# Kernel optimization log

Hardware: AMD Instinct MI355X
Metric: run time of the kernel (lower is better)

## Reference

```python
import jax, jax.numpy as jnp
import numpy as np

B, N, F, D, TOPK, EXTRA = 32, 128, 10, 64, 20, 25
BN = B * N
EPS = 1e-5
SLOPE = 0.2  # GDN GraphLayer leaky_relu negative slope


def _cosine(a, b):
    na = jnp.maximum(jnp.linalg.norm(a, axis=-1), 1e-12)
    nb = jnp.maximum(jnp.linalg.norm(b, axis=-1), 1e-12)
    return (a @ b.T) / (na[:, None] * nb[None, :])


def _segment_softmax(logits, seg, num):
    m = jax.ops.segment_max(logits, seg, num_segments=num)
    m = jnp.where(jnp.isfinite(m), m, 0.0)  # empty segments
    e = jnp.exp(logits - m[seg])
    s = jax.ops.segment_sum(e, seg, num_segments=num)
    return e / jnp.maximum(s[seg], 1e-12)


def setup_inputs() -> dict:
    key = jax.random.key(0)
    ks = jax.random.split(key, 12)
    r = lambda i, shape, s=1.0: jax.random.normal(ks[i], shape, dtype=jnp.float32) * s
    return dict(
        data=r(0, (B, N, F)),
        emb=r(1, (N, D)) * 0.3,                       # nn.Embedding(node_num, dim)
        W1=r(2, (F, D)) * (1.0 / np.sqrt(F)),         # GraphLayer lin
        att_i1=r(3, (2 * D,)) * 0.1,                  # att on concat(h, emb)
        att_j1=r(4, (2 * D,)) * 0.1,
        bias1=jnp.zeros((D,), jnp.float32),
        bn1_g=jnp.ones((D,), jnp.float32),
        bn1_b=jnp.zeros((D,), jnp.float32),
        P=r(5, (BN, BN)) * (1.0 / np.sqrt(BN)),       # extra_pram
        W2=r(6, (D, D)) * (1.0 / np.sqrt(D)),         # GraphLayer1 lin
        att_i2=r(7, (D,)) * 0.1,
        att_j2=r(8, (D,)) * 0.1,
        bias2=jnp.zeros((D,), jnp.float32),
        bnO_g=jnp.ones((D,), jnp.float32),
        bnO_b=jnp.zeros((D,), jnp.float32),
        W_out=r(9, (D, 1)) * (1.0 / np.sqrt(D)),      # OutLayer Linear(dim,1)
        b_out=jnp.zeros((1,), jnp.float32),
        org_edge_index=jnp.zeros((2, 2), jnp.int32),  # dead arg in original forward
    )


def _forward(data, emb, W1, att_i1, att_j1, bias1, bn1_g, bn1_b, P, W2,
             att_i2, att_j2, bias2, bnO_g, bnO_b, W_out, b_out):
    x = data.reshape(BN, F)

    # ---- learned top-k graph from detached embedding cosine similarity ----
    w = jax.lax.stop_gradient(emb)              # weights_arr = detach()
    cos = _cosine(w, w)                         # [N, N]
    topv, topi = jax.lax.top_k(cos, TOPK)       # [N, TOPK]
    cos_w = jnp.tile(topv.reshape(-1), B)       # [B*N*TOPK]
    src0 = topi.reshape(-1)                     # gated_j (source)
    dst0 = jnp.repeat(jnp.arange(N), TOPK)      # gated_i (target)
    offs = jnp.repeat(jnp.arange(B) * N, N * TOPK)
    src = jnp.tile(src0, B) + offs
    dst = jnp.tile(dst0, B) + offs

    # ---- GraphLayer (GAT-style with embedding keys, edge weight = cos) ----
    all_emb = jnp.tile(emb, (B, 1))             # [BN, D]
    h = x @ W1                                  # [BN, D]
    kf = jnp.concatenate([h, all_emb], axis=-1) # [BN, 2D]
    si, sj = kf @ att_i1, kf @ att_j1           # [BN]
    score = jax.nn.leaky_relu(si[dst] + sj[src], SLOPE) * cos_w
    alpha = _segment_softmax(score, dst, BN)
    agg = jax.ops.segment_sum(h[src] * alpha[:, None], dst, num_segments=BN) + bias1
    mu, var = agg.mean(0), agg.var(0)           # BatchNorm1d (batch stats)
    gcn = jax.nn.relu(bn1_g * (agg - mu) / jnp.sqrt(var + EPS) + bn1_b)

    # ---- extra-feature branch (always taken: P is [BN, BN]) ----
    ef = P.T @ gcn                              # (gcn_out.T @ P).T
    g = jnp.concatenate([gcn, ef], axis=0)      # [2BN, D]
    cos2 = _cosine(g, g)                        # [2BN, 2BN]
    topv2, topi2 = jax.lax.top_k(cos2, EXTRA)
    corrs = topv2[:BN].reshape(-1)              # [BN*EXTRA]
    src2 = jnp.repeat(jnp.arange(BN), EXTRA)    # extra_i = edge_index[0] (source)
    dst2 = topi2[:BN].reshape(-1)               # extra_j = edge_index[1] (target)

    # ---- GraphLayer1 (no embedding keys, no BN in GNNLayer1.forward) ----
    h2 = g @ W2                                 # [2BN, D]
    s2 = jax.nn.leaky_relu((h2 @ att_i2)[dst2] + (h2 @ att_j2)[src2], SLOPE) * corrs
    alpha2 = _segment_softmax(s2, dst2, 2 * BN)
    agg2 = jax.ops.segment_sum(h2[src2] * alpha2[:, None], dst2, num_segments=2 * BN) + bias2
    gcn2 = jax.nn.relu(agg2)[:BN]

    # ---- output head: mul by embedding, BN over channels, Linear(D,1) ----
    x3 = gcn2.reshape(B, N, D) * emb[None]      # [B, N, D]
    mu2, var2 = x3.mean((0, 1)), x3.var((0, 1)) # BatchNorm1d over channel D
    x4 = jax.nn.relu(bnO_g * (x3 - mu2) / jnp.sqrt(var2 + EPS) + bnO_b)
    out = x4 @ W_out + b_out                    # [B, N, 1]; dropout = identity (eval)
    return out.reshape(-1, N)                   # [B, N]


def reference(data, emb, W1, att_i1, att_j1, bias1, bn1_g, bn1_b, P, W2,
              att_i2, att_j2, bias2, bnO_g, bnO_b, W_out, b_out, org_edge_index):
    # org_edge_index is dead in the original forward (only cached, never consumed)
    return _forward(data, emb, W1, att_i1, att_j1, bias1, bn1_g, bn1_b, P, W2,
                    att_i2, att_j2, bias2, bnO_g, bnO_b, W_out, b_out)
```

## Files before the change

kernel.cpp:

```cpp
#include <hip/hip_runtime.h>
#include <hip/hip_bf16.h>
#include <math.h>

#define DEV __device__ __forceinline__

constexpr int Bb   = 32;
constexpr int Nn   = 128;
constexpr int Ff   = 10;
constexpr int Dd   = 64;
constexpr int TOPK = 20;
constexpr int EXTRA= 25;
constexpr int BN   = 4096;
constexpr int TBN  = 8192;
constexpr int RC   = 16;
constexpr int CAND_CAP = 1024;
constexpr float EPS   = 1e-5f;
constexpr float SLOPE = 0.2f;

DEV unsigned int fenc(float f){
  unsigned int b = __float_as_uint(f);
  return (b & 0x80000000u) ? ~b : (b | 0x80000000u);
}
DEV float fdec(unsigned int u){
  unsigned int b = (u & 0x80000000u) ? (u & 0x7FFFFFFFu) : ~u;
  return __uint_as_float(b);
}

__global__ void k_zero(float* __restrict__ p, int n){
  int i = blockIdx.x*256 + threadIdx.x;
  if(i < n) p[i] = 0.f;
}

__global__ void k_emb_norm(const float* __restrict__ emb, float* __restrict__ norms){
  int i = blockIdx.x, d = threadIdx.x;
  float v = emb[i*Dd + d];
  float s = v*v;
  for(int o=32;o>0;o>>=1) s += __shfl_down(s, o, 64);
  if(d==0) norms[i] = fmaxf(sqrtf(s), 1e-12f);
}

__global__ void k_emb_topk(const float* __restrict__ emb, const float* __restrict__ norms,
                           float* __restrict__ topv, int* __restrict__ topi){
  __shared__ float se[Dd];
  __shared__ float sc[Nn];
  __shared__ float rv[Nn];
  __shared__ int   ri[Nn];
  int i = blockIdx.x, t = threadIdx.x;
  if(t < Dd) se[t] = emb[i*Dd + t];
  __syncthreads();
  float dot = 0.f;
  for(int d=0; d<Dd; d++) dot += se[d]*emb[t*Dd + d];
  sc[t] = dot/(norms[i]*norms[t]);
  __syncthreads();
  for(int k=0; k<TOPK; k++){
    rv[t] = sc[t]; ri[t] = t; __syncthreads();
    for(int o=Nn/2; o>0; o>>=1){
      if(t < o){
        float v2 = rv[t+o]; int i2 = ri[t+o];
        if(v2 > rv[t] || (v2 == rv[t] && i2 < ri[t])){ rv[t]=v2; ri[t]=i2; }
      }
      __syncthreads();
    }
    if(t==0){
      topv[i*TOPK + k] = rv[0];
      topi[i*TOPK + k] = ri[0];
      sc[ri[0]] = -INFINITY;
    }
    __syncthreads();
  }
}

__global__ void k_h1(const float* __restrict__ data, const float* __restrict__ emb,
                     const float* __restrict__ W1, const float* __restrict__ ai1,
                     const float* __restrict__ aj1,
                     float* __restrict__ h, float* __restrict__ si, float* __restrict__ sj){
  int r = blockIdx.x, d = threadIdx.x;
  int node = r & (Nn-1);
  __shared__ float xr[Ff];
  if(d < Ff) xr[d] = data[r*Ff + d];
  __syncthreads();
  float hv = 0.f;
  #pragma unroll
  for(int f=0; f<Ff; f++) hv += xr[f]*W1[f*Dd + d];
  h[r*Dd + d] = hv;
  float e = emb[node*Dd + d];
  float a = hv*ai1[d] + e*ai1[Dd + d];
  float b = hv*aj1[d] + e*aj1[Dd + d];
  for(int o=32;o>0;o>>=1){ a += __shfl_down(a,o,64); b += __shfl_down(b,o,64); }
  if(d==0){ si[r] = a; sj[r] = b; }
}

__global__ void k_agg1(const float* __restrict__ h, const float* __restrict__ si,
                       const float* __restrict__ sj, const float* __restrict__ topv,
                       const int* __restrict__ topi, const float* __restrict__ bias1,
                       float* __restrict__ agg){
  int r = blockIdx.x, d = threadIdx.x;
  int b = r >> 7, node = r & (Nn-1);
  __shared__ float sal[TOPK];
  __shared__ int   ssrc[TOPK];
  if(d < TOPK){
    int s = b*Nn + topi[node*TOPK + d];
    float sc = si[r] + sj[s];
    sc = sc >= 0.f ? sc : SLOPE*sc;
    sal[d] = sc * topv[node*TOPK + d];
    ssrc[d] = s;
  }
  __syncthreads();
  float m = -INFINITY;
  #pragma unroll
  for(int k=0;k<TOPK;k++) m = fmaxf(m, sal[k]);
  float al[TOPK]; float ssum = 0.f;
  #pragma unroll
  for(int k=0;k<TOPK;k++){ al[k] = expf(sal[k]-m); ssum += al[k]; }
  float inv = 1.0f/fmaxf(ssum, 1e-12f);
  float acc = 0.f;
  #pragma unroll
  for(int k=0;k<TOPK;k++) acc += al[k]*inv*h[ssrc[k]*Dd + d];
  agg[r*Dd + d] = acc + bias1[d];
}

__global__ void k_colstats(const float* __restrict__ x, float* __restrict__ mu, float* __restrict__ var){
  int c = blockIdx.x, t = threadIdx.x;
  float s = 0.f, s2 = 0.f;
  for(int r=t; r<BN; r+=256){ float v = x[r*Dd + c]; s += v; s2 += v*v; }
  __shared__ float ls[256], ls2[256];
  ls[t]=s; ls2[t]=s2; __syncthreads();
  for(int o=128;o>0;o>>=1){
    if(t<o){ ls[t]+=ls[t+o]; ls2[t]+=ls2[t+o]; }
    __syncthreads();
  }
  if(t==0){ float m = ls[0]/BN; mu[c]=m; var[c]=ls2[0]/BN - m*m; }
}

__global__ void k_bnrelu1(const float* __restrict__ agg, const float* __restrict__ mu,
                          const float* __restrict__ var, const float* __restrict__ gamma,
                          const float* __restrict__ beta, float* __restrict__ g){
  int idx = blockIdx.x*256 + threadIdx.x;
  int c = idx & (Dd-1);
  float v = agg[idx];
  float y = gamma[c]*(v - mu[c])/sqrtf(var[c]+EPS) + beta[c];
  g[idx] = fmaxf(y, 0.f);
}

__global__ __launch_bounds__(256) void k_ef1(const float* __restrict__ P, const float* __restrict__ gcn,
                                             float* __restrict__ part){
  __shared__ float Pt[16*64];
  __shared__ float Gt[16*64];
  int t = threadIdx.x;
  int jbase = blockIdx.x*64;
  int r0 = blockIdx.y*256;
  int row = t >> 4, col4 = (t & 15)*4;
  int tr = t >> 4, tc = t & 15;
  float acc[4][4] = {};
  for(int step=0; step<16; step++){
    int r = r0 + step*16;
    float4 pv = *(const float4*)&P[(size_t)(r+row)*BN + jbase + col4];
    float4 gv = *(const float4*)&gcn[(r+row)*Dd + col4];
    __syncthreads();
    *(float4*)&Pt[row*64 + col4] = pv;
    *(float4*)&Gt[row*64 + col4] = gv;
    __syncthreads();
    #pragma unroll
    for(int rr=0; rr<16; rr++){
      float4 pa = *(float4*)&Pt[rr*64 + tr*4];
      float4 gb = *(float4*)&Gt[rr*64 + tc*4];
      float pav[4] = {pa.x, pa.y, pa.z, pa.w};
      float gbv[4] = {gb.x, gb.y, gb.z, gb.w};
      #pragma unroll
      for(int a=0;a<4;a++)
        #pragma unroll
        for(int b=0;b<4;b++) acc[a][b] += pav[a]*gbv[b];
    }
  }
  float* dst = part + ((size_t)blockIdx.y*BN + jbase)*Dd;
  #pragma unroll
  for(int a=0;a<4;a++){
    float4 v = make_float4(acc[a][0],acc[a][1],acc[a][2],acc[a][3]);
    *(float4*)&dst[(tr*4+a)*Dd + tc*4] = v;
  }
}

__global__ void k_ef2(const float* __restrict__ part, float* __restrict__ ef){
  int i = blockIdx.x*256 + threadIdx.x;
  float4 s = make_float4(0.f,0.f,0.f,0.f);
  #pragma unroll
  for(int c=0;c<RC;c++){
    float4 v = *(const float4*)&part[(size_t)c*BN*Dd + (size_t)i*4];
    s.x += v.x; s.y += v.y; s.z += v.z; s.w += v.w;
  }
  *(float4*)&ef[(size_t)i*4] = s;
}

__global__ void k_rownorm(const float* __restrict__ x, float* __restrict__ nrm){
  int r = blockIdx.x, d = threadIdx.x;
  float v = x[(size_t)r*Dd + d];
  float s = v*v;
  for(int o=32;o>0;o>>=1) s += __shfl_down(s, o, 64);
  if(d==0) nrm[r] = fmaxf(sqrtf(s), 1e-12f);
}

__global__ __launch_bounds__(256) void k_sgemm(const float* __restrict__ g, const float* __restrict__ gnorm,
                                               int rbase, float* __restrict__ S){
  __shared__ float A[64*128];
  __shared__ float Bs[64*128];
  int t = threadIdx.x;
  int ctile = blockIdx.x*128;
  int rtile = rbase + blockIdx.y*128;
  int q = t >> 4, m0 = t & 15;
  #pragma unroll
  for(int l=0;l<8;l++){
    int m = m0 + 16*l;
    float ia = 1.0f/gnorm[rtile + m];
    float ib = 1.0f/gnorm[ctile + m];
    float4 av = *(const float4*)&g[(size_t)(rtile+m)*Dd + q*4];
    float4 bv = *(const float4*)&g[(size_t)(ctile+m)*Dd + q*4];
    A[(q*4+0)*128 + m] = av.x*ia; A[(q*4+1)*128 + m] = av.y*ia;
    A[(q*4+2)*128 + m] = av.z*ia; A[(q*4+3)*128 + m] = av.w*ia;
    Bs[(q*4+0)*128 + m] = bv.x*ib; Bs[(q*4+1)*128 + m] = bv.y*ib;
    Bs[(q*4+2)*128 + m] = bv.z*ib; Bs[(q*4+3)*128 + m] = bv.w*ib;
  }
  __syncthreads();
  int tr = t >> 4;
  int tc = t & 15;
  float acc[8][8] = {};
  #pragma unroll 4
  for(int k=0;k<64;k++){
    float a[8], b[8];
    #pragma unroll
    for(int i=0;i<8;i++) a[i] = A[k*128 + tr + 16*i];
    #pragma unroll
    for(int j=0;j<8;j++) b[j] = Bs[k*128 + tc + 16*j];
    #pragma unroll
    for(int i=0;i<8;i++)
      #pragma unroll
      for(int j=0;j<8;j++) acc[i][j] += a[i]*b[j];
  }
  int rloc = blockIdx.y*128;
  #pragma unroll
  for(int i=0;i<8;i++){
    int r = rloc + tr + 16*i;
    #pragma unroll
    for(int j=0;j<8;j++)
      S[(size_t)r*TBN + ctile + tc + 16*j] = acc[i][j];
  }
}

__global__ __launch_bounds__(256) void k_radix(const float* __restrict__ S, int rbase,
                                               float* __restrict__ topv2, int* __restrict__ topi2){
  __shared__ unsigned hist[4096];
  __shared__ unsigned wtot[4];
  __shared__ unsigned candE[CAND_CAP];
  __shared__ unsigned short candC[CAND_CAP];
  __shared__ unsigned bc_bin, bc_need, bc_cnt, bc_c;
  int t = threadIdx.x;
  int lane = t & 63, wid = t >> 6;
  int r = blockIdx.x;
  const float* src = S + (size_t)r*TBN;
  int col0 = t*32;
  unsigned enc[32];
  #pragma unroll
  for(int j=0;j<8;j++){
    float4 v = *(const float4*)&src[col0 + j*4];
    enc[j*4+0]=fenc(v.x); enc[j*4+1]=fenc(v.y); enc[j*4+2]=fenc(v.z); enc[j*4+3]=fenc(v.w);
  }
  #pragma unroll
  for(int j=0;j<16;j++) hist[t*16 + j] = 0u;
  __syncthreads();
  #pragma unroll
  for(int j=0;j<32;j++) atomicAdd(&hist[enc[j] >> 20], 1u);
  __syncthreads();
  unsigned lsum = 0u;
  #pragma unroll
  for(int j=0;j<16;j++) lsum += hist[t*16 + j];
  unsigned v = lsum;
  #pragma unroll
  for(int o=1;o<64;o<<=1){
    unsigned u = (unsigned)__shfl_down((int)v, o, 64);
    if(lane + o < 64) v += u;
  }
  if(lane == 0) wtot[wid] = v;
  __syncthreads();
  unsigned cross = 0u;
  #pragma unroll
  for(int w2=0;w2<4;w2++) if(w2 > wid) cross += wtot[w2];
  unsigned Tinc = v + cross;
  unsigned above = Tinc - lsum;
  unsigned run = above;
  #pragma unroll
  for(int b=15;b>=0;b--){
    unsigned prev = run;
    run += hist[t*16 + b];
    if(run >= EXTRA && prev < EXTRA){ bc_bin = (unsigned)(t*16 + b); bc_need = EXTRA - prev; }
  }
  if(t==0){ bc_cnt = 0u; bc_c = 0u; }
  __syncthreads();
  unsigned pivotBin = bc_bin, needIn = bc_need;
  int gr = rbase + r;
  #pragma unroll
  for(int j=0;j<32;j++){
    unsigned e = enc[j];
    unsigned bin = e >> 20;
    if(bin > pivotBin){
      unsigned s = atomicAdd(&bc_cnt, 1u);
      topv2[gr*EXTRA + s] = fdec(e);
      topi2[gr*EXTRA + s] = col0 + j;
    } else if(bin == pivotBin){
      unsigned ci = atomicAdd(&bc_c, 1u);
      if(ci < CAND_CAP){ candE[ci] = e; candC[ci] = (unsigned short)(col0 + j); }
    }
  }
  __syncthreads();
  unsigned c = bc_c;
  if(c <= CAND_CAP){
    for(unsigned i=t; i<c; i+=256){
      unsigned ei = candE[i]; unsigned coli = candC[i];
      unsigned rank = 0;
      for(unsigned j2=0;j2<c;j2++){
        unsigned ej = candE[j2];
        rank += (ej > ei) || (ej == ei && candC[j2] < coli);
      }
      if(rank < needIn){
        unsigned s = atomicAdd(&bc_cnt, 1u);
        topv2[gr*EXTRA + s] = fdec(ei);
        topi2[gr*EXTRA + s] = (int)coli;
      }
    }
  } else {
    unsigned* h256  = hist;
    unsigned* scanb = hist + 1024;
    unsigned prefix = pivotBin;
    unsigned need = needIn;
    const int shifts[3] = {12, 4, 0};
    const unsigned masks[3] = {255u, 255u, 15u};
    const int nbins[3] = {256, 256, 16};
    for(int p=0;p<3;p++){
      int sh = shifts[p]; unsigned mk = masks[p]; int nb = nbins[p];
      if(t < nb) h256[t] = 0u;
      __syncthreads();
      #pragma unroll
      for(int j=0;j<32;j++){
        unsigned e = enc[j];
        int pshift = (p==0)? 20 : (p==1? 12 : 4);
        if((e >> pshift) == prefix) atomicAdd(&h256[(e>>sh)&mk], 1u);
      }
      __syncthreads();
      unsigned vv = (t < nb) ? h256[t] : 0u;
      for(int o=1;o<nb;o<<=1){
        if(t < nb) scanb[t] = vv;
        __syncthreads();
        if(t < nb && t+o < nb) vv += scanb[t+o];
        __syncthreads();
      }
      if(t < nb) scanb[t] = vv;
      __syncthreads();
      if(t < nb){
        unsigned nxt = (t < nb-1) ? scanb[t+1] : 0u;
        if(vv >= need && nxt < need){ bc_bin = (prefix << ((p==2)?4:8)) | (unsigned)t; bc_need = need - nxt; }
      }
      __syncthreads();
      prefix = bc_bin; need = bc_need;
      __syncthreads();
    }
    unsigned pivotEnc = prefix;
    unsigned needTies = need;
    unsigned tie_local = 0u;
    #pragma unroll
    for(int j=0;j<32;j++){
      unsigned e = enc[j];
      if((e >> 20) == pivotBin){
        if(e > pivotEnc){
          unsigned s = atomicAdd(&bc_cnt, 1u);
          topv2[gr*EXTRA + s] = fdec(e);
          topi2[gr*EXTRA + s] = col0 + j;
        } else if(e == pivotEnc) tie_local++;
      }
    }
    unsigned iv = tie_local;
    for(int o=1;o<256;o<<=1){
      scanb[t] = iv; __syncthreads();
      if(t >= o) iv += scanb[t-o];
      __syncthreads();
    }
    unsigned rank = iv - tie_local;
    #pragma unroll
    for(int j=0;j<32;j++){
      unsigned e = enc[j];
      if(e == pivotEnc && (e >> 20) == pivotBin){
        if(rank < needTies){
          unsigned s = atomicAdd(&bc_cnt, 1u);
          topv2[gr*EXTRA + s] = fdec(e);
          topi2[gr*EXTRA + s] = col0 + j;
        }
        rank++;
      }
    }
  }
}

__global__ void k_h2(const float* __restrict__ g, const float* __restrict__ W2,
                     const float* __restrict__ ai2w, const float* __restrict__ aj2w,
                     float* __restrict__ h2, float* __restrict__ a2i, float* __restrict__ a2j){
  int r = blockIdx.x, d = threadIdx.x;
  __shared__ float gr[Dd];
  gr[d] = g[(size_t)r*Dd + d];
  __syncthreads();
  float hv = 0.f;
  #pragma unroll
  for(int k=0;k<Dd;k++) hv += gr[k]*W2[k*Dd + d];
  h2[(size_t)r*Dd + d] = hv;
  float a = hv*ai2w[d];
  float b = hv*aj2w[d];
  for(int o=32;o>0;o>>=1){ a += __shfl_down(a,o,64); b += __shfl_down(b,o,64); }
  if(d==0){ a2i[r]=a; a2j[r]=b; }
}

__global__ void k_s2(const float* __restrict__ a2i, const float* __restrict__ a2j,
                     const float* __restrict__ topv2, const int* __restrict__ topi2,
                     float* __restrict__ s2, unsigned int* __restrict__ segmax){
  int e = blockIdx.x*256 + threadIdx.x;
  if(e >= BN*EXTRA) return;
  int r = e/EXTRA;
  int dst = topi2[e];
  float sc = a2i[dst] + a2j[r];
  sc = sc >= 0.f ? sc : SLOPE*sc;
  sc *= topv2[e];
  s2[e] = sc;
  atomicMax(&segmax[dst], fenc(sc));
}

__global__ void k_e2(const float* __restrict__ s2, const int* __restrict__ topi2,
                     const unsigned int* __restrict__ segmax,
                     float* __restrict__ e2, float* __restrict__ ssum){
  int e = blockIdx.x*256 + threadIdx.x;
  if(e >= BN*EXTRA) return;
  int dst = topi2[e];
  float m = fdec(segmax[dst]);
  float v = expf(s2[e] - m);
  e2[e] = v;
  atomicAdd(&ssum[dst], v);
}

__global__ void k_scat(const float* __restrict__ e2, const float* __restrict__ ssum,
                       const int* __restrict__ topi2, const float* __restrict__ h2,
                       float* __restrict__ agg2){
  int idx = blockIdx.x*256 + threadIdx.x;
  int e = idx >> 6, d = idx & 63;
  int dst = topi2[e];
  int src = e/EXTRA;
  float alpha = e2[e]/fmaxf(ssum[dst], 1e-12f);
  atomicAdd(&agg2[(size_t)dst*Dd + d], alpha*h2[(size_t)src*Dd + d]);
}

__global__ void k_headstats(const float* __restrict__ agg2, const float* __restrict__ bias2,
                            const float* __restrict__ emb, float* __restrict__ mu2, float* __restrict__ var2){
  int c = blockIdx.x, t = threadIdx.x;
  float bc = bias2[c];
  float s = 0.f, s2 = 0.f;
  for(int r=t; r<BN; r+=256){
    float v = fmaxf(agg2[(size_t)r*Dd + c] + bc, 0.f) * emb[(r & (Nn-1))*Dd + c];
    s += v; s2 += v*v;
  }
  __shared__ float ls[256], ls2[256];
  ls[t]=s; ls2[t]=s2; __syncthreads();
  for(int o=128;o>0;o>>=1){
    if(t<o){ ls[t]+=ls[t+o]; ls2[t]+=ls2[t+o]; }
    __syncthreads();
  }
  if(t==0){ float m=ls[0]/BN; mu2[c]=m; var2[c]=ls2[0]/BN - m*m; }
}

__global__ void k_out(const float* __restrict__ agg2, const float* __restrict__ bias2,
                      const float* __restrict__ emb, const float* __restrict__ mu2,
                      const float* __restrict__ var2, const float* __restrict__ gO,
                      const float* __restrict__ bO, const float* __restrict__ Wout,
                      const float* __restrict__ bout, float* __restrict__ out){
  int r = blockIdx.x, d = threadIdx.x;
  float v = fmaxf(agg2[(size_t)r*Dd + d] + bias2[d], 0.f) * emb[(r & (Nn-1))*Dd + d];
  float y = gO[d]*(v - mu2[d])/sqrtf(var2[d]+EPS) + bO[d];
  y = fmaxf(y, 0.f)*Wout[d];
  for(int o=32;o>0;o>>=1) y += __shfl_down(y, o, 64);
  if(d==0) out[r] = y + bout[0];
}

extern "C" void kernel_launch(void* const* d_in, const int* in_sizes, int n_in,
                              void* d_out, int out_size, void* d_ws, size_t ws_size,
                              hipStream_t stream){
  const float* data  = (const float*)d_in[0];
  const float* emb   = (const float*)d_in[1];
  const float* W1    = (const float*)d_in[2];
  const float* ai1   = (const float*)d_in[3];
  const float* aj1   = (const float*)d_in[4];
  const float* bias1 = (const float*)d_in[5];
  const float* bn1g  = (const float*)d_in[6];
  const float* bn1b  = (const float*)d_in[7];
  const float* P     = (const float*)d_in[8];
  const float* W2    = (const float*)d_in[9];
  const float* ai2w  = (const float*)d_in[10];
  const float* aj2w  = (const float*)d_in[11];
  const float* bias2 = (const float*)d_in[12];
  const float* bnOg  = (const float*)d_in[13];
  const float* bnOb  = (const float*)d_in[14];
  const float* Wout  = (const float*)d_in[15];
  const float* bout  = (const float*)d_in[16];
  float* out = (float*)d_out;

  char* w = (char*)d_ws;
  auto alloc = [&](size_t nbytes)->char*{
    char* p = w; w += (nbytes + 255) & ~(size_t)255; return p;
  };
  float* norms1 = (float*)alloc(Nn*4);
  float* topv1  = (float*)alloc(Nn*TOPK*4);
  int*   topi1  = (int*)  alloc(Nn*TOPK*4);
  float* h      = (float*)alloc((size_t)BN*Dd*4);
  float* si     = (float*)alloc(BN*4);
  float* sj     = (float*)alloc(BN*4);
  float* agg1   = (float*)alloc((size_t)BN*Dd*4);
  float* mu1    = (float*)alloc(Dd*4);
  float* var1   = (float*)alloc(Dd*4);
  float* g      = (float*)alloc((size_t)TBN*Dd*4);
  float* gnorm  = (float*)alloc(TBN*4);
  float* topv2  = (float*)alloc((size_t)BN*EXTRA*4);
  int*   topi2  = (int*)  alloc((size_t)BN*EXTRA*4);
  float* h2     = (float*)alloc((size_t)TBN*Dd*4);
  float* a2i    = (float*)alloc(TBN*4);
  float* a2j    = (float*)alloc(TBN*4);
  float* s2     = (float*)alloc((size_t)BN*EXTRA*4);
  float* e2     = (float*)alloc((size_t)BN*EXTRA*4);
  float* zblock = (float*)alloc(((size_t)TBN*Dd + TBN + TBN)*4);
  float* agg2   = zblock;
  float* ssum   = zblock + (size_t)TBN*Dd;
  unsigned int* segmax = (unsigned int*)(ssum + TBN);
  float* mu2    = (float*)alloc(Dd*4);
  float* var2   = (float*)alloc(Dd*4);
  float* efpart = (float*)alloc((size_t)RC*BN*Dd*4);

  size_t used = (size_t)(w - (char*)d_ws);
  size_t rem  = ws_size > used ? ws_size - used : 0;
  int chunkRows = 4096;
  while(chunkRows > 128 && (size_t)chunkRows*TBN*4 > rem) chunkRows >>= 1;
  float* Schunk = (float*)alloc((size_t)chunkRows*TBN*4);

  k_emb_norm<<<Nn, 64, 0, stream>>>(emb, norms1);
  k_emb_topk<<<Nn, Nn, 0, stream>>>(emb, norms1, topv1, topi1);
  k_h1<<<BN, 64, 0, stream>>>(data, emb, W1, ai1, aj1, h, si, sj);
  k_agg1<<<BN, 64, 0, stream>>>(h, si, sj, topv1, topi1, bias1, agg1);
  k_colstats<<<Dd, 256, 0, stream>>>(agg1, mu1, var1);
  k_bnrelu1<<<(BN*Dd)/256, 256, 0, stream>>>(agg1, mu1, var1, bn1g, bn1b, g);

  k_ef1<<<dim3(64, RC), 256, 0, stream>>>(P, g, efpart);
  k_ef2<<<(BN*Dd/4)/256, 256, 0, stream>>>(efpart, g + (size_t)BN*Dd);

  k_rownorm<<<TBN, 64, 0, stream>>>(g, gnorm);
  for(int rbase=0; rbase<BN; rbase+=chunkRows){
    k_sgemm<<<dim3(TBN/128, chunkRows/128), 256, 0, stream>>>(g, gnorm, rbase, Schunk);
    k_radix<<<chunkRows, 256, 0, stream>>>(Schunk, rbase, topv2, topi2);
  }

  k_h2<<<TBN, 64, 0, stream>>>(g, W2, ai2w, aj2w, h2, a2i, a2j);
  k_zero<<<((TBN*Dd + 2*TBN) + 255)/256, 256, 0, stream>>>(zblock, TBN*Dd + 2*TBN);
  k_s2<<<(BN*EXTRA + 255)/256, 256, 0, stream>>>(a2i, a2j, topv2, topi2, s2, segmax);
  k_e2<<<(BN*EXTRA + 255)/256, 256, 0, stream>>>(s2, topi2, segmax, e2, ssum);
  k_scat<<<(BN*EXTRA*Dd)/256, 256, 0, stream>>>(e2, ssum, topi2, h2, agg2);

  k_headstats<<<Dd, 256, 0, stream>>>(agg2, bias2, emb, mu2, var2);
  k_out<<<BN, 64, 0, stream>>>(agg2, bias2, emb, mu2, var2, bnOg, bnOb, Wout, bout, out);
}
```

Measured before the change: 387.4 us.

## Compute cosine similarity GEMM with bf16x3 split MFMA instead of FP32 FMA

Row normalization now also splits each normalized row into three bf16 parts (high, mid, low). The similarity GEMM is recomputed with 16x16x32 bf16 MFMA instructions, accumulating six cross products to keep near-FP32 accuracy. Operands are loaded directly from global memory into registers, replacing the LDS-staged scalar FMA tile. This is meant to move the 4096x8192x64 GEMM onto matrix cores, at the cost of extra MFMA work, triple-size operand buffers, and possible small accuracy differences that could alter top-k selection.

```diff
diff --git a/kernel.cpp b/kernel.cpp
--- a/kernel.cpp
+++ b/kernel.cpp
@@ -17,6 +17,9 @@
 constexpr float EPS   = 1e-5f;
 constexpr float SLOPE = 0.2f;
 
+typedef __attribute__((ext_vector_type(8))) short bf16x8;
+typedef __attribute__((ext_vector_type(4))) float f32x4;
+
 DEV unsigned int fenc(float f){
   unsigned int b = __float_as_uint(f);
   return (b & 0x80000000u) ? ~b : (b | 0x80000000u);
@@ -24,6 +27,15 @@
 DEV float fdec(unsigned int u){
   unsigned int b = (u & 0x80000000u) ? (u & 0x7FFFFFFFu) : ~u;
   return __uint_as_float(b);
+}
+
+DEV unsigned short f2bf(float f){
+  unsigned u = __float_as_uint(f);
+  u += 0x7FFFu + ((u >> 16) & 1u);
+  return (unsigned short)(u >> 16);
+}
+DEV float bf2f(unsigned short h){
+  return __uint_as_float(((unsigned)h) << 16);
 }
 
 __global__ void k_zero(float* __restrict__ p, int n){
@@ -191,57 +203,95 @@
   *(float4*)&ef[(size_t)i*4] = s;
 }
 
-__global__ void k_rownorm(const float* __restrict__ x, float* __restrict__ nrm){
+__global__ void k_gn(const float* __restrict__ x,
+                     unsigned short* __restrict__ gh,
+                     unsigned short* __restrict__ gm,
+                     unsigned short* __restrict__ gl){
   int r = blockIdx.x, d = threadIdx.x;
   float v = x[(size_t)r*Dd + d];
   float s = v*v;
   for(int o=32;o>0;o>>=1) s += __shfl_down(s, o, 64);
-  if(d==0) nrm[r] = fmaxf(sqrtf(s), 1e-12f);
-}
-
-__global__ __launch_bounds__(256) void k_sgemm(const float* __restrict__ g, const float* __restrict__ gnorm,
+  s = __shfl(s, 0, 64);
+  float inv = 1.0f/fmaxf(sqrtf(s), 1e-12f);
+  float vn = v*inv;
+  unsigned short h = f2bf(vn);
+  float r1 = vn - bf2f(h);
+  unsigned short m = f2bf(r1);
+  float r2 = r1 - bf2f(m);
+  unsigned short l = f2bf(r2);
+  size_t idx = (size_t)r*Dd + d;
+  gh[idx] = h; gm[idx] = m; gl[idx] = l;
+}
+
+__global__ __launch_bounds__(256) void k_sgemm(const unsigned short* __restrict__ gh,
+                                               const unsigned short* __restrict__ gm,
+                                               const unsigned short* __restrict__ gl,
                                                int rbase, float* __restrict__ S){
-  __shared__ float A[64*128];
-  __shared__ float Bs[64*128];
   int t = threadIdx.x;
+  int w = t >> 6, l = t & 63;
+  int lr = l & 15;
+  int kq = l >> 4;
   int ctile = blockIdx.x*128;
-  int rtile = rbase + blockIdx.y*128;
-  int q = t >> 4, m0 = t & 15;
-  #pragma unroll
-  for(int l=0;l<8;l++){
-    int m = m0 + 16*l;
-    float ia = 1.0f/gnorm[rtile + m];
-    float ib = 1.0f/gnorm[ctile + m];
-    float4 av = *(const float4*)&g[(size_t)(rtile+m)*Dd + q*4];
-    float4 bv = *(const float4*)&g[(size_t)(ctile+m)*Dd + q*4];
-    A[(q*4+0)*128 + m] = av.x*ia; A[(q*4+1)*128 + m] = av.y*ia;
-    A[(q*4+2)*128 + m] = av.z*ia; A[(q*4+3)*128 + m] = av.w*ia;
-    Bs[(q*4+0)*128 + m] = bv.x*ib; Bs[(q*4+1)*128 + m] = bv.y*ib;
-    Bs[(q*4+2)*128 + m] = bv.z*ib; Bs[(q*4+3)*128 + m] = bv.w*ib;
-  }
-  __syncthreads();
-  int tr = t >> 4;
-  int tc = t & 15;
-  float acc[8][8] = {};
-  #pragma unroll 4
-  for(int k=0;k<64;k++){
-    float a[8], b[8];
+  int rtile0 = rbase + blockIdx.y*128 + w*32;
+
+  bf16x8 ah[2][2], am[2][2], alo[2][2];
+  #pragma unroll
+  for(int m=0;m<2;m++){
+    size_t rowoff = (size_t)(rtile0 + m*16 + lr)*Dd;
     #pragma unroll
-    for(int i=0;i<8;i++) a[i] = A[k*128 + tr + 16*i];
+    for(int kh=0;kh<2;kh++){
+      size_t off = rowoff + kh*32 + kq*8;
+      ah[m][kh]  = *(const bf16x8*)(gh + off);
+      am[m][kh]  = *(const bf16x8*)(gm + off);
+      alo[m][kh] = *(const bf16x8*)(gl + off);
+    }
+  }
+  f32x4 acc[2][8];
+  #pragma unroll
+  for(int m=0;m<2;m++)
     #pragma unroll
-    for(int j=0;j<8;j++) b[j] = Bs[k*128 + tc + 16*j];
+    for(int n=0;n<8;n++)
+      acc[m][n] = (f32x4){0.f,0.f,0.f,0.f};
+
+  #pragma unroll
+  for(int n=0;n<8;n++){
+    size_t coloff = (size_t)(ctile + n*16 + lr)*Dd;
+    bf16x8 bh0 = *(const bf16x8*)(gh + coloff + kq*8);
+    bf16x8 bh1 = *(const bf16x8*)(gh + coloff + 32 + kq*8);
+    bf16x8 bm0 = *(const bf16x8*)(gm + coloff + kq*8);
+    bf16x8 bm1 = *(const bf16x8*)(gm + coloff + 32 + kq*8);
+    bf16x8 bl0 = *(const bf16x8*)(gl + coloff + kq*8);
+    bf16x8 bl1 = *(const bf16x8*)(gl + coloff + 32 + kq*8);
     #pragma unroll
-    for(int i=0;i<8;i++)
+    for(int m=0;m<2;m++){
+      f32x4 c = acc[m][n];
+      c = __builtin_amdgcn_mfma_f32_16x16x32_bf16(ah[m][0], bh0, c, 0,0,0);
+      c = __builtin_amdgcn_mfma_f32_16x16x32_bf16(ah[m][1], bh1, c, 0,0,0);
+      c = __builtin_amdgcn_mfma_f32_16x16x32_bf16(ah[m][0], bm0, c, 0,0,0);
+      c = __builtin_amdgcn_mfma_f32_16x16x32_bf16(ah[m][1], bm1, c, 0,0,0);
+      c = __builtin_amdgcn_mfma_f32_16x16x32_bf16(am[m][0], bh0, c, 0,0,0);
+      c = __builtin_amdgcn_mfma_f32_16x16x32_bf16(am[m][1], bh1, c, 0,0,0);
+      c = __builtin_amdgcn_mfma_f32_16x16x32_bf16(ah[m][0], bl0, c, 0,0,0);
+      c = __builtin_amdgcn_mfma_f32_16x16x32_bf16(ah[m][1], bl1, c, 0,0,0);
+      c = __builtin_amdgcn_mfma_f32_16x16x32_bf16(alo[m][0], bh0, c, 0,0,0);
+      c = __builtin_amdgcn_mfma_f32_16x16x32_bf16(alo[m][1], bh1, c, 0,0,0);
+      c = __builtin_amdgcn_mfma_f32_16x16x32_bf16(am[m][0], bm0, c, 0,0,0);
+      c = __builtin_amdgcn_mfma_f32_16x16x32_bf16(am[m][1], bm1, c, 0,0,0);
+      acc[m][n] = c;
+    }
+  }
+
+  int rloc = blockIdx.y*128 + w*32;
+  #pragma unroll
+  for(int m=0;m<2;m++){
+    #pragma unroll
+    for(int j=0;j<4;j++){
+      int row = rloc + m*16 + kq*4 + j;
       #pragma unroll
-      for(int j=0;j<8;j++) acc[i][j] += a[i]*b[j];
-  }
-  int rloc = blockIdx.y*128;
-  #pragma unroll
-  for(int i=0;i<8;i++){
-    int r = rloc + tr + 16*i;
-    #pragma unroll
-    for(int j=0;j<8;j++)
-      S[(size_t)r*TBN + ctile + tc + 16*j] = acc[i][j];
+      for(int n=0;n<8;n++){
+        S[(size_t)row*TBN + ctile + n*16 + lr] = acc[m][n][j];
+      }
+    }
   }
 }
 
@@ -518,7 +568,9 @@
   float* mu1    = (float*)alloc(Dd*4);
   float* var1   = (float*)alloc(Dd*4);
   float* g      = (float*)alloc((size_t)TBN*Dd*4);
-  float* gnorm  = (float*)alloc(TBN*4);
+  unsigned short* gnh = (unsigned short*)alloc((size_t)TBN*Dd*2);
+  unsigned short* gnm = (unsigned short*)alloc((size_t)TBN*Dd*2);
+  unsigned short* gnl = (unsigned short*)alloc((size_t)TBN*Dd*2);
   float* topv2  = (float*)alloc((size_t)BN*EXTRA*4);
   int*   topi2  = (int*)  alloc((size_t)BN*EXTRA*4);
   float* h2     = (float*)alloc((size_t)TBN*Dd*4);
@@ -550,9 +602,9 @@
   k_ef1<<<dim3(64, RC), 256, 0, stream>>>(P, g, efpart);
   k_ef2<<<(BN*Dd/4)/256, 256, 0, stream>>>(efpart, g + (size_t)BN*Dd);
 
-  k_rownorm<<<TBN, 64, 0, stream>>>(g, gnorm);
+  k_gn<<<TBN, 64, 0, stream>>>(g, gnh, gnm, gnl);
   for(int rbase=0; rbase<BN; rbase+=chunkRows){
-    k_sgemm<<<dim3(TBN/128, chunkRows/128), 256, 0, stream>>>(g, gnorm, rbase, Schunk);
+    k_sgemm<<<dim3(TBN/128, chunkRows/128), 256, 0, stream>>>(gnh, gnm, gnl, rbase, Schunk);
     k_radix<<<chunkRows, 256, 0, stream>>>(Schunk, rbase, topv2, topi2);
   }
 
```

Measured after the change: 385.0 us. About the same (-0.6%).
